# Performance work log

Measured on AMD Instinct MI355X. Metric: run time of the kernel, lower is better.

Reference implementation:

```python
import jax, jax.numpy as jnp
import numpy as np

N, E, G = 50000, 500000, 2000   # nodes, edges, graphs
IN, H, ED, OUT = 64, 128, 16, 1
NUM_GAT = 2                      # num_layers - 1
T = 2                            # num_timesteps


def leaky(x, s=0.01):
    return jnp.where(x >= 0, x, s * x)


def gru_cell(x, h, wih, whh, bih, bhh):
    gi = x @ wih.T + bih
    gh = h @ whh.T + bhh
    ir, iz, inn = jnp.split(gi, 3, -1)
    hr, hz, hn = jnp.split(gh, 3, -1)
    r = jax.nn.sigmoid(ir + hr)
    z = jax.nn.sigmoid(iz + hz)
    n = jnp.tanh(inn + r * hn)
    return (1.0 - z) * n + z * h


def lstm_cell(x, h, c, wih, whh, bih, bhh):
    g = x @ wih.T + bih + h @ whh.T + bhh
    i, f, gg, o = jnp.split(g, 4, -1)
    c2 = jax.nn.sigmoid(f) * c + jax.nn.sigmoid(i) * jnp.tanh(gg)
    h2 = jax.nn.sigmoid(o) * jnp.tanh(c2)
    return h2, c2


def setup_inputs() -> dict:
    key = jax.random.key(0)
    ks = iter(jax.random.split(key, 40))
    def rn(shape, s=0.05):
        return jax.random.normal(next(ks), shape, jnp.float32) * s
    return {
        "x": jax.random.normal(next(ks), (N, IN), jnp.float32),
        "edge_index": jax.random.randint(next(ks), (2, E), 0, N),
        "edge_attr": jax.random.normal(next(ks), (E, ED), jnp.float32),
        "batch": jnp.sort(jax.random.randint(next(ks), (N,), 0, G)),
        "lin1_w": rn((H, IN)), "lin1_b": rn((H,)),
        "nd_lin1_w": rn((H, H + ED)), "nd_lin2_w": rn((H, H)), "nd_bias": rn((H,)),
        "gru0_wih": rn((3 * H, H)), "gru0_whh": rn((3 * H, H)),
        "gru0_bih": rn((3 * H,)), "gru0_bhh": rn((3 * H,)),
        "gat_w": rn((NUM_GAT, H, H)), "gat_asrc": rn((NUM_GAT, H)),
        "gat_adst": rn((NUM_GAT, H)), "gat_b": rn((NUM_GAT, H)),
        "gru_wih": rn((NUM_GAT, 3 * H, H)), "gru_whh": rn((NUM_GAT, 3 * H, H)),
        "gru_bih": rn((NUM_GAT, 3 * H)), "gru_bhh": rn((NUM_GAT, 3 * H)),
        "gin_w": rn((H, H)), "gin_b": rn((H,)),
        "lstm_wih": rn((4 * H, H)), "lstm_whh": rn((4 * H, H)),
        "lstm_bih": rn((4 * H,)), "lstm_bhh": rn((4 * H,)),
        "lin2_w": rn((OUT, H)), "lin2_b": rn((OUT,)),
    }


def reference(x, edge_index, edge_attr, batch,
              lin1_w, lin1_b, nd_lin1_w, nd_lin2_w, nd_bias,
              gru0_wih, gru0_whh, gru0_bih, gru0_bhh,
              gat_w, gat_asrc, gat_adst, gat_b,
              gru_wih, gru_whh, gru_bih, gru_bhh,
              gin_w, gin_b, lstm_wih, lstm_whh, lstm_bih, lstm_bhh,
              lin2_w, lin2_b):
    src, dst = edge_index[0], edge_index[1]  # PyG: messages flow src(j) -> dst(i)
    # input projection
    x1 = leaky(x @ lin1_w.T + lin1_b)
    # nd_conv: gather -> MLP -> scatter-add (dropout=0 in eval)
    m = leaky(jnp.concatenate([x1[src], edge_attr], -1) @ nd_lin1_w.T) @ nd_lin2_w.T
    h = jax.nn.elu(jax.ops.segment_sum(m, dst, num_segments=N) + nd_bias)
    xcur = jax.nn.relu(gru_cell(h, x1, gru0_wih, gru0_whh, gru0_bih, gru0_bhh))
    # GAT layers (heads=1, no self loops, negative_slope=0.01)
    for l in range(NUM_GAT):
        xp = xcur @ gat_w[l].T
        a = leaky(xp[src] @ gat_asrc[l] + xp[dst] @ gat_adst[l], 0.01)
        amax = jax.lax.stop_gradient(jax.ops.segment_max(a, dst, num_segments=N))
        ae = jnp.exp(a - amax[dst])
        denom = jax.ops.segment_sum(ae, dst, num_segments=N)
        alpha = ae / denom[dst]
        h = jax.nn.elu(jax.ops.segment_sum(alpha[:, None] * xp[src], dst, num_segments=N) + gat_b[l])
        xcur = jax.nn.relu(gru_cell(h, xcur,
                                    gru_wih[l], gru_whh[l], gru_bih[l], gru_bhh[l]))
    # global readout: GIN on bipartite (nodes -> graphs) + LSTM refinement
    agg = jax.ops.segment_sum(xcur, batch, num_segments=G)  # [G, H], constant over timesteps
    out = jax.nn.relu(agg)
    for _ in range(T):
        h = jax.nn.elu((out + agg) @ gin_w.T + gin_b)  # GIN eps=0: nn(x_dst + aggr)
        out, _ = lstm_cell(out, h, h, lstm_wih, lstm_whh, lstm_bih, lstm_bhh)
    return out @ lin2_w.T + lin2_b  # [G, OUT]
```

## Files before the change

### kernel.cpp

```cpp
#include <hip/hip_runtime.h>
#include <cstdint>
#include <cmath>

#define NN 50000
#define EE 500000
#define GG 2000

#define DEV __device__ __forceinline__

typedef __attribute__((ext_vector_type(8))) short short8;
typedef __attribute__((ext_vector_type(4))) float floatx4;
typedef _Float16 half2v __attribute__((ext_vector_type(2)));
typedef _Float16 half4v __attribute__((ext_vector_type(4)));
typedef _Float16 half8v __attribute__((ext_vector_type(8)));

DEV float fsig(float x) { return 1.f / (1.f + __expf(-x)); }
DEV float ftanh(float x) {
    const float e = __expf(-2.f * fabsf(x));
    const float t = (1.f - e) / (1.f + e);
    return x >= 0.f ? t : -t;
}

DEV float actf(float x, int act) {
    if (act == 1) return x >= 0.f ? x : 0.01f * x;
    if (act == 2) return x > 0.f ? x : __expf(x) - 1.f;
    if (act == 3) return x > 0.f ? x : 0.f;
    return x;
}

DEV float hdot2(half2v a, half2v b, float c) {
#if __has_builtin(__builtin_amdgcn_fdot2)
    return __builtin_amdgcn_fdot2(a, b, c, false);
#else
    return c + (float)a[0] * (float)b[0] + (float)a[1] * (float)b[1];
#endif
}

#define H2(v, i) __builtin_shufflevector(v, v, 2 * (i), 2 * (i) + 1)

__global__ __launch_bounds__(256) void gemm_f16_k(
    const _Float16* __restrict__ A, const _Float16* __restrict__ W,
    const float* __restrict__ bias, _Float16* __restrict__ C,
    int M, int K, int Nout, int act)
{
    __shared__ unsigned short Als[64 * 136];
    __shared__ unsigned short Bls[64 * 136];
    const int tid = threadIdx.x;
    const int bm = blockIdx.y * 64;
    const int bn = blockIdx.x * 64;

    const int ks = (K == 128) ? 7 : 6;
    const int km = K - 1;
    const int nch = (64 * K) >> 3;
    for (int i = tid; i < nch; i += 256) {
        const int e8 = i << 3;
        const int r = e8 >> ks;
        const int c = e8 & km;
        short8 av = {};
        if (bm + r < M) av = *(const short8*)(A + (size_t)(bm + r) * K + c);
        *(short8*)(Als + r * 136 + c) = av;
        *(short8*)(Bls + r * 136 + c) = *(const short8*)(W + (size_t)(bn + r) * K + c);
    }
    __syncthreads();

    const int wave = tid >> 6;
    const int lane = tid & 63;
    const int wr = (wave >> 1) * 32;
    const int wc = (wave & 1) * 32;
    const int l15 = lane & 15;
    const int quad = lane >> 4;

    floatx4 acc00 = {}, acc01 = {}, acc10 = {}, acc11 = {};
    for (int k0 = 0; k0 < K; k0 += 32) {
        const half8v a0 = *(const half8v*)(Als + (wr + l15) * 136 + k0 + quad * 8);
        const half8v a1 = *(const half8v*)(Als + (wr + 16 + l15) * 136 + k0 + quad * 8);
        const half8v b0 = *(const half8v*)(Bls + (wc + l15) * 136 + k0 + quad * 8);
        const half8v b1 = *(const half8v*)(Bls + (wc + 16 + l15) * 136 + k0 + quad * 8);
        acc00 = __builtin_amdgcn_mfma_f32_16x16x32_f16(a0, b0, acc00, 0, 0, 0);
        acc01 = __builtin_amdgcn_mfma_f32_16x16x32_f16(a0, b1, acc01, 0, 0, 0);
        acc10 = __builtin_amdgcn_mfma_f32_16x16x32_f16(a1, b0, acc10, 0, 0, 0);
        acc11 = __builtin_amdgcn_mfma_f32_16x16x32_f16(a1, b1, acc11, 0, 0, 0);
    }

    const floatx4* accs[4] = { &acc00, &acc01, &acc10, &acc11 };
#pragma unroll
    for (int r = 0; r < 2; ++r) {
#pragma unroll
        for (int c = 0; c < 2; ++c) {
            const floatx4 a = *accs[r * 2 + c];
            const int n = bn + wc + c * 16 + l15;
            const float bv = bias ? bias[n] : 0.f;
#pragma unroll
            for (int i = 0; i < 4; ++i) {
                const int m = bm + wr + r * 16 + quad * 4 + i;
                if (m < M) C[(size_t)m * Nout + n] = (_Float16)actf(a[i] + bv, act);
            }
        }
    }
}

__global__ __launch_bounds__(256) void gemm_dots_k(
    const _Float16* __restrict__ A, const _Float16* __restrict__ W,
    _Float16* __restrict__ C, const float* __restrict__ asrc,
    const float* __restrict__ adst, float* __restrict__ ssrc,
    float* __restrict__ sdst, int M)
{
    __shared__ unsigned short Als[64 * 136];
    __shared__ unsigned short Bls[64 * 136];
    const int tid = threadIdx.x;
    const int bm = blockIdx.y * 64;
    const int bn = blockIdx.x * 64;

    for (int i = tid; i < 1024; i += 256) {
        const int e8 = i << 3;
        const int r = e8 >> 7;
        const int c = e8 & 127;
        short8 av = {};
        if (bm + r < M) av = *(const short8*)(A + (size_t)(bm + r) * 128 + c);
        *(short8*)(Als + r * 136 + c) = av;
        *(short8*)(Bls + r * 136 + c) = *(const short8*)(W + (size_t)(bn + r) * 128 + c);
    }
    __syncthreads();

    const int wave = tid >> 6;
    const int lane = tid & 63;
    const int wr = (wave >> 1) * 32;
    const int wc = (wave & 1) * 32;
    const int l15 = lane & 15;
    const int quad = lane >> 4;

    floatx4 acc00 = {}, acc01 = {}, acc10 = {}, acc11 = {};
    for (int k0 = 0; k0 < 128; k0 += 32) {
        const half8v a0 = *(const half8v*)(Als + (wr + l15) * 136 + k0 + quad * 8);
        const half8v a1 = *(const half8v*)(Als + (wr + 16 + l15) * 136 + k0 + quad * 8);
        const half8v b0 = *(const half8v*)(Bls + (wc + l15) * 136 + k0 + quad * 8);
        const half8v b1 = *(const half8v*)(Bls + (wc + 16 + l15) * 136 + k0 + quad * 8);
        acc00 = __builtin_amdgcn_mfma_f32_16x16x32_f16(a0, b0, acc00, 0, 0, 0);
        acc01 = __builtin_amdgcn_mfma_f32_16x16x32_f16(a0, b1, acc01, 0, 0, 0);
        acc10 = __builtin_amdgcn_mfma_f32_16x16x32_f16(a1, b0, acc10, 0, 0, 0);
        acc11 = __builtin_amdgcn_mfma_f32_16x16x32_f16(a1, b1, acc11, 0, 0, 0);
    }

    const floatx4* accs[4] = { &acc00, &acc01, &acc10, &acc11 };
#pragma unroll
    for (int r = 0; r < 2; ++r)
#pragma unroll
        for (int c = 0; c < 2; ++c) {
            const floatx4 a = *accs[r * 2 + c];
            const int n = bn + wc + c * 16 + l15;
#pragma unroll
            for (int i = 0; i < 4; ++i) {
                const int m = bm + wr + r * 16 + quad * 4 + i;
                if (m < M) C[(size_t)m * 128 + n] = (_Float16)a[i];
            }
        }

    const int n0 = bn + wc + l15;
    const int n1 = n0 + 16;
    const float as0 = asrc[n0], as1 = asrc[n1];
    const float ad0 = adst[n0], ad1 = adst[n1];
#pragma unroll
    for (int r = 0; r < 2; ++r) {
        const floatx4 a0 = r ? acc10 : acc00;
        const floatx4 a1 = r ? acc11 : acc01;
#pragma unroll
        for (int i = 0; i < 4; ++i) {
            float vs = a0[i] * as0 + a1[i] * as1;
            float vd = a0[i] * ad0 + a1[i] * ad1;
            vs += __shfl_down(vs, 8, 16);
            vs += __shfl_down(vs, 4, 16);
            vs += __shfl_down(vs, 2, 16);
            vs += __shfl_down(vs, 1, 16);
            vd += __shfl_down(vd, 8, 16);
            vd += __shfl_down(vd, 4, 16);
            vd += __shfl_down(vd, 2, 16);
            vd += __shfl_down(vd, 1, 16);
            const int m = bm + wr + r * 16 + quad * 4 + i;
            if (l15 == 0 && m < M) {
                atomicAdd(ssrc + m, vs);
                atomicAdd(sdst + m, vd);
            }
        }
    }
}

__global__ __launch_bounds__(256) void lin1p_k(
    const _Float16* __restrict__ xH, const _Float16* __restrict__ lin1_wH,
    const float* __restrict__ lin1_b, const _Float16* __restrict__ nd1wAH,
    _Float16* __restrict__ x1H, _Float16* __restrict__ pH, int M)
{
    __shared__ _Float16 sXin[64 * 72];
    __shared__ _Float16 sX1 [64 * 136];
    const int tid = threadIdx.x;
    const int bm = blockIdx.x * 64;

    for (int i = tid; i < 512; i += 256) {
        const int e8 = i << 3;
        const int r = e8 >> 6;
        const int c = e8 & 63;
        const int m = bm + r;
        half8v v = {};
        if (m < M) v = *(const half8v*)(xH + (size_t)m * 64 + c);
        *(half8v*)(sXin + r * 72 + c) = v;
    }
    __syncthreads();

    const int wave = tid >> 6, lane = tid & 63;
    const int l15 = lane & 15, quad = lane >> 4;
    const int wr = (wave >> 1) * 32;
    const int wc = (wave & 1) * 64;

    {
        floatx4 acc[2][4] = {};
#pragma unroll
        for (int k = 0; k < 2; ++k) {
            half8v a[2];
#pragma unroll
            for (int rf = 0; rf < 2; ++rf)
                a[rf] = *(const half8v*)(sXin + (wr + rf * 16 + l15) * 72 + k * 32 + quad * 8);
#pragma unroll
            for (int ct = 0; ct < 4; ++ct) {
                const half8v b = *(const half8v*)(lin1_wH + (size_t)(wc + ct * 16 + l15) * 64 + k * 32 + quad * 8);
#pragma unroll
                for (int rf = 0; rf < 2; ++rf)
                    acc[rf][ct] = __builtin_amdgcn_mfma_f32_16x16x32_f16(a[rf], b, acc[rf][ct], 0, 0, 0);
            }
        }
#pragma unroll
        for (int rf = 0; rf < 2; ++rf)
#pragma unroll
            for (int ct = 0; ct < 4; ++ct) {
                const int n = wc + ct * 16 + l15;
                const float bv = lin1_b[n];
#pragma unroll
                for (int i = 0; i < 4; ++i) {
                    const int rloc = wr + rf * 16 + quad * 4 + i;
                    float v = acc[rf][ct][i] + bv;
                    v = v >= 0.f ? v : 0.01f * v;
                    const _Float16 h = (_Float16)v;
                    sX1[rloc * 136 + n] = h;
                    const int m = bm + rloc;
                    if (m < M) x1H[(size_t)m * 128 + n] = h;
                }
            }
    }
    __syncthreads();

    {
        floatx4 acc[2][4] = {};
#pragma unroll
        for (int k = 0; k < 4; ++k) {
            half8v a[2];
#pragma unroll
            for (int rf = 0; rf < 2; ++rf)
                a[rf] = *(const half8v*)(sX1 + (wr + rf * 16 + l15) * 136 + k * 32 + quad * 8);
#pragma unroll
            for (int ct = 0; ct < 4; ++ct) {
                const half8v b = *(const half8v*)(nd1wAH + (size_t)(wc + ct * 16 + l15) * 128 + k * 32 + quad * 8);
#pragma unroll
                for (int rf = 0; rf < 2; ++rf)
                    acc[rf][ct] = __builtin_amdgcn_mfma_f32_16x16x32_f16(a[rf], b, acc[rf][ct], 0, 0, 0);
            }
        }
#pragma unroll
        for (int rf = 0; rf < 2; ++rf)
#pragma unroll
            for (int ct = 0; ct < 4; ++ct) {
                const int n = wc + ct * 16 + l15;
#pragma unroll
                for (int i = 0; i < 4; ++i) {
                    const int m = bm + wr + rf * 16 + quad * 4 + i;
                    if (m < M) pH[(size_t)m * 128 + n] = (_Float16)acc[rf][ct][i];
                }
            }
    }
}

__global__ __launch_bounds__(256, 4) void gru_fused4_k(
    const _Float16* __restrict__ xin, const _Float16* __restrict__ hin,
    const _Float16* __restrict__ wih, const _Float16* __restrict__ whh,
    const float* __restrict__ bih, const float* __restrict__ bhh,
    _Float16* __restrict__ xout, int M)
{
    __shared__ unsigned short sX[64 * 136];
    __shared__ unsigned short sH[64 * 136];

    const int tid = threadIdx.x;
    const int bm = blockIdx.x * 64;

    for (int i = tid; i < 1024; i += 256) {
        const int e8 = i << 3;
        const int r = e8 >> 7;
        const int c = e8 & 127;
        const int m = bm + r;
        short8 xv = {}, hv = {};
        if (m < M) {
            xv = *(const short8*)(xin + (size_t)m * 128 + c);
            hv = *(const short8*)(hin + (size_t)m * 128 + c);
        }
        *(short8*)(sX + r * 136 + c) = xv;
        *(short8*)(sH + r * 136 + c) = hv;
    }
    __syncthreads();

    const int wave = tid >> 6;
    const int lane = tid & 63;
    const int l15 = lane & 15;
    const int quad = lane >> 4;
    const int j0 = (blockIdx.y * 4 + wave) * 16;
    const int j = j0 + l15;

    const float br  = bih[j] + bhh[j];
    const float bz  = bih[128 + j] + bhh[128 + j];
    const float bni = bih[256 + j];
    const float bnh = bhh[256 + j];

    floatx4 aR[4] = {}, aZ[4] = {}, aNi[4] = {}, aNh[4] = {};

#pragma unroll
    for (int k = 0; k < 4; ++k) {
        const size_t wrow = (size_t)(j0 + l15) * 128 + k * 32 + quad * 8;
        const half8v wri = *(const half8v*)(wih + wrow);
        const half8v wzi = *(const half8v*)(wih + 128 * 128 + wrow);
        const half8v wni = *(const half8v*)(wih + 2 * 128 * 128 + wrow);
        const half8v wrh = *(const half8v*)(whh + wrow);
        const half8v wzh = *(const half8v*)(whh + 128 * 128 + wrow);
        const half8v wnh = *(const half8v*)(whh + 2 * 128 * 128 + wrow);
#pragma unroll
        for (int rf = 0; rf < 4; ++rf) {
            const half8v ax = *(const half8v*)(sX + (rf * 16 + l15) * 136 + k * 32 + quad * 8);
            const half8v ah = *(const half8v*)(sH + (rf * 16 + l15) * 136 + k * 32 + quad * 8);
            aR[rf]  = __builtin_amdgcn_mfma_f32_16x16x32_f16(ax, wri, aR[rf], 0, 0, 0);
            aR[rf]  = __builtin_amdgcn_mfma_f32_16x16x32_f16(ah, wrh, aR[rf], 0, 0, 0);
            aZ[rf]  = __builtin_amdgcn_mfma_f32_16x16x32_f16(ax, wzi, aZ[rf], 0, 0, 0);
            aZ[rf]  = __builtin_amdgcn_mfma_f32_16x16x32_f16(ah, wzh, aZ[rf], 0, 0, 0);
            aNi[rf] = __builtin_amdgcn_mfma_f32_16x16x32_f16(ax, wni, aNi[rf], 0, 0, 0);
            aNh[rf] = __builtin_amdgcn_mfma_f32_16x16x32_f16(ah, wnh, aNh[rf], 0, 0, 0);
        }
    }

#pragma unroll
    for (int rf = 0; rf < 4; ++rf) {
#pragma unroll
        for (int i = 0; i < 4; ++i) {
            const int m = bm + rf * 16 + quad * 4 + i;
            if (m >= M) continue;
            const float rg = fsig(aR[rf][i] + br);
            const float zg = fsig(aZ[rf][i] + bz);
            const float ng = ftanh(aNi[rf][i] + bni + rg * (aNh[rf][i] + bnh));
            const float hp = (float)((const _Float16*)sH)[(rf * 16 + quad * 4 + i) * 136 + j];
            const float v = (1.f - zg) * ng + zg * hp;
            xout[(size_t)m * 128 + j] = (_Float16)(v > 0.f ? v : 0.f);
        }
    }
}

__global__ void hist_k(const int* __restrict__ ei, int* __restrict__ deg, int E)
{
    int e = blockIdx.x * 256 + threadIdx.x;
    if (e >= E) return;
    atomicAdd(deg + ei[E + e], 1);
}

__global__ __launch_bounds__(1024) void scan_part_k(const int* __restrict__ deg,
                                                    int* __restrict__ bsum, int n)
{
    __shared__ int sh[1024];
    const int t = threadIdx.x;
    const int i = blockIdx.x * 1024 + t;
    sh[t] = (i < n) ? deg[i] : 0;
    __syncthreads();
#pragma unroll
    for (int off = 512; off; off >>= 1) {
        if (t < off) sh[t] += sh[t + off];
        __syncthreads();
    }
    if (t == 0) bsum[blockIdx.x] = sh[0];
}

__global__ void scan_tops_k(const int* __restrict__ bsum, int* __restrict__ boff,
                            int nb, int* __restrict__ rowptr, int n)
{
    if (threadIdx.x != 0 || blockIdx.x != 0) return;
    int run = 0;
    for (int b = 0; b < nb; ++b) { boff[b] = run; run += bsum[b]; }
    rowptr[n] = run;
}

__global__ __launch_bounds__(1024) void scan_final_k(const int* __restrict__ deg,
                                                     const int* __restrict__ boff,
                                                     int* __restrict__ rowptr, int n)
{
    __shared__ int sh[1024];
    const int t = threadIdx.x;
    const int i = blockIdx.x * 1024 + t;
    const int v = (i < n) ? deg[i] : 0;
    sh[t] = v;
    __syncthreads();
#pragma unroll
    for (int off = 1; off < 1024; off <<= 1) {
        int add = (t >= off) ? sh[t - off] : 0;
        __syncthreads();
        sh[t] += add;
        __syncthreads();
    }
    if (i < n) rowptr[i] = boff[blockIdx.x] + sh[t] - v;
}

__global__ void fill_csr_k(const int* __restrict__ ei, const int* __restrict__ rowptr,
                           int* __restrict__ cursor, int* __restrict__ csr_src,
                           int* __restrict__ csr_eid, int E)
{
    int e = blockIdx.x * 256 + threadIdx.x;
    if (e >= E) return;
    int s = ei[e], d = ei[E + e];
    int pos = atomicAdd(cursor + d, 1);
    int slot = rowptr[d] + pos;
    csr_src[slot] = s;
    csr_eid[slot] = e;
}

__global__ void gptr_k(const int* __restrict__ batch, int* __restrict__ gptr,
                       int N, int G)
{
    int n = blockIdx.x * 256 + threadIdx.x;
    if (n >= N) return;
    if (n == 0) {
        for (int g = 0; g <= batch[0]; ++g) gptr[g] = 0;
    } else {
        const int a = batch[n - 1], b = batch[n];
        for (int g = a + 1; g <= b; ++g) gptr[g] = n;
    }
    if (n == N - 1) {
        for (int g = batch[N - 1] + 1; g <= G; ++g) gptr[g] = N;
    }
}

__global__ __launch_bounds__(128) void graph_sum_k(
    const _Float16* __restrict__ xc, const int* __restrict__ gptr,
    _Float16* __restrict__ aggH)
{
    const int g = blockIdx.x;
    const int t = threadIdx.x;
    const int n0 = gptr[g], n1 = gptr[g + 1];
    float acc = 0.f;
    for (int n = n0; n < n1; ++n) acc += (float)xc[(size_t)n * 128 + t];
    aggH[(size_t)g * 128 + t] = (_Float16)acc;
}

struct CvtSeg { const float* src; _Float16* dst; int n; };
struct CvtArgs { CvtSeg s[12]; int count; };

__global__ void cvt_multi_k(CvtArgs a)
{
    const int seg = blockIdx.y;
    if (seg >= a.count) return;
    const CvtSeg cs = a.s[seg];
    for (int i = blockIdx.x * 256 + threadIdx.x; i < cs.n; i += gridDim.x * 256)
        cs.dst[i] = (_Float16)cs.src[i];
}

__global__ void cvt_ndwA_k(const float* __restrict__ ndw, _Float16* __restrict__ outp)
{
    int t = blockIdx.x * 256 + threadIdx.x;
    if (t >= 16384) return;
    int r = t >> 7, c = t & 127;
    outp[r * 128 + c] = (_Float16)ndw[r * 144 + c];
}

__global__ void cvt_ndwB_k(const float* __restrict__ ndw, _Float16* __restrict__ outp)
{
    int t = blockIdx.x * 256 + threadIdx.x;
    if (t >= 2048) return;
    int r = t >> 4, k = t & 15;
    outp[r * 16 + k] = (_Float16)ndw[r * 144 + 128 + k];
}

__global__ __launch_bounds__(128) void nd_gather_k(
    const int* __restrict__ rowptr, const int* __restrict__ csr_src,
    const int* __restrict__ csr_eid, const _Float16* __restrict__ eaH,
    const _Float16* __restrict__ wH, const _Float16* __restrict__ pH,
    _Float16* __restrict__ outp)
{
    __shared__ float racc[4][128];
    const int d = blockIdx.x;
    const int t = threadIdx.x;
    const int g  = t >> 5;
    const int fq = t & 31;

    half8v w0[4], w1[4];
#pragma unroll
    for (int f = 0; f < 4; ++f) {
        w0[f] = *(const half8v*)(wH + (fq * 4 + f) * 16);
        w1[f] = *(const half8v*)(wH + (fq * 4 + f) * 16 + 8);
    }

    const int b0 = rowptr[d], b1 = rowptr[d + 1];
    float acc[4] = {};
    for (int i = b0 + g; i < b1; i += 4) {
        const int s = csr_src[i], e = csr_eid[i];
        const half8v e0 = *(const half8v*)(eaH + (size_t)e * 16);
        const half8v e1 = *(const half8v*)(eaH + (size_t)e * 16 + 8);
        const half4v p4 = *(const half4v*)(pH + (size_t)s * 128 + fq * 4);
#pragma unroll
        for (int f = 0; f < 4; ++f) {
            float q = 0.f;
            q = hdot2(H2(e0, 0), H2(w0[f], 0), q);
            q = hdot2(H2(e0, 1), H2(w0[f], 1), q);
            q = hdot2(H2(e0, 2), H2(w0[f], 2), q);
            q = hdot2(H2(e0, 3), H2(w0[f], 3), q);
            q = hdot2(H2(e1, 0), H2(w1[f], 0), q);
            q = hdot2(H2(e1, 1), H2(w1[f], 1), q);
            q = hdot2(H2(e1, 2), H2(w1[f], 2), q);
            q = hdot2(H2(e1, 3), H2(w1[f], 3), q);
            const float v = (float)p4[f] + q;
            acc[f] += v >= 0.f ? v : 0.01f * v;
        }
    }
#pragma unroll
    for (int f = 0; f < 4; ++f) racc[g][fq * 4 + f] = acc[f];
    __syncthreads();

    outp[(size_t)d * 128 + t] =
        (_Float16)(racc[0][t] + racc[1][t] + racc[2][t] + racc[3][t]);
}

__global__ __launch_bounds__(128) void gat_gather_k(
    const int* __restrict__ rowptr, const int* __restrict__ csr_src,
    const float* __restrict__ ssrc, const float* __restrict__ sdst,
    const _Float16* __restrict__ xp, const float* __restrict__ bias,
    _Float16* __restrict__ outp)
{
    const int d = blockIdx.x;
    const int t = threadIdx.x;
    __shared__ float red[128];
    __shared__ float lw[128];
    __shared__ int   ls[128];
    __shared__ float racc[4][128];

    const int b0 = rowptr[d], b1 = rowptr[d + 1];
    const int deg = b1 - b0;
    const float sdd = sdst[d];

    const int g  = t >> 5;
    const int fq = t & 31;
    float4 acc = make_float4(0.f, 0.f, 0.f, 0.f);
    float dpart = 0.f;
    for (int base = b0; base < b1; base += 128) {
        const int len = min(128, b1 - base);
        if (t < len) {
            const int s = csr_src[base + t];
            float a = ssrc[s] + sdd;
            a = a >= 0.f ? a : 0.01f * a;
            const float w = __expf(a);
            lw[t] = w;
            ls[t] = s;
            dpart += w;
        }
        __syncthreads();
        for (int j = 0; j < len; j += 4) {
            const int jj = j + g;
            if (jj < len) {
                const float w = lw[jj];
                const half4v hv = *(const half4v*)(xp + (size_t)ls[jj] * 128 + fq * 4);
                acc.x += w * (float)hv[0];
                acc.y += w * (float)hv[1];
                acc.z += w * (float)hv[2];
                acc.w += w * (float)hv[3];
            }
        }
        __syncthreads();
    }

    red[t] = dpart;
    __syncthreads();
#pragma unroll
    for (int off = 64; off; off >>= 1) {
        if (t < off) red[t] += red[t + off];
        __syncthreads();
    }
    const float denom = red[0];

    racc[g][fq * 4 + 0] = acc.x;
    racc[g][fq * 4 + 1] = acc.y;
    racc[g][fq * 4 + 2] = acc.z;
    racc[g][fq * 4 + 3] = acc.w;
    __syncthreads();

    const float s4 = racc[0][t] + racc[1][t] + racc[2][t] + racc[3][t];
    float v = (deg > 0 ? s4 / denom : 0.f) + bias[t];
    outp[(size_t)d * 128 + t] = (_Float16)(v > 0.f ? v : __expf(v) - 1.f);
}

__global__ __launch_bounds__(256) void gin_lstm_k(
    const _Float16* __restrict__ aggH,
    const _Float16* __restrict__ ginw, const float* __restrict__ ginb,
    const _Float16* __restrict__ lwih, const _Float16* __restrict__ lwhh,
    const float* __restrict__ lbih, const float* __restrict__ lbhh,
    const float* __restrict__ l2w, const float* __restrict__ l2b,
    float* __restrict__ y, int G)
{
    __shared__ _Float16 sOa[16 * 136];
    __shared__ _Float16 sOb[16 * 136];
    __shared__ _Float16 sG [16 * 136];
    __shared__ _Float16 sT [16 * 136];
    __shared__ float    sC [16 * 128];

    const int tid = threadIdx.x, wave = tid >> 6, lane = tid & 63;
    const int l15 = lane & 15, quad = lane >> 4;
    const int g0 = blockIdx.x * 16;

    {
        const int r = tid >> 4;
        const int c = (tid & 15) * 8;
        half8v v = {};
        if (g0 + r < G) v = *(const half8v*)(aggH + (size_t)(g0 + r) * 128 + c);
        *(half8v*)(sG + r * 136 + c) = v;
        half8v rv;
#pragma unroll
        for (int i = 0; i < 8; ++i) rv[i] = (float)v[i] > 0.f ? v[i] : (_Float16)0.f;
        *(half8v*)(sOa + r * 136 + c) = rv;
    }
    __syncthreads();

    _Float16* sIn = sOa;
    _Float16* sOut = sOb;
#pragma unroll
    for (int ts = 0; ts < 2; ++ts) {
        for (int ci = 0; ci < 2; ++ci) {
            const int j0 = (wave * 2 + ci) * 16;
            floatx4 acc = {};
#pragma unroll
            for (int k = 0; k < 4; ++k) {
                const half8v b = *(const half8v*)(ginw + (size_t)(j0 + l15) * 128 + k * 32 + quad * 8);
                const half8v a = *(const half8v*)(sIn + l15 * 136 + k * 32 + quad * 8)
                               + *(const half8v*)(sG  + l15 * 136 + k * 32 + quad * 8);
                acc = __builtin_amdgcn_mfma_f32_16x16x32_f16(a, b, acc, 0, 0, 0);
            }
            const int j = j0 + l15;
            const float bg = ginb[j];
#pragma unroll
            for (int i = 0; i < 4; ++i) {
                const int row = quad * 4 + i;
                float v = acc[i] + bg;
                v = v > 0.f ? v : __expf(v) - 1.f;
                sT[row * 136 + j] = (_Float16)v;
                sC[row * 128 + j] = v;
            }
        }
        __syncthreads();

        for (int ci = 0; ci < 2; ++ci) {
            const int j0 = (wave * 2 + ci) * 16;
            floatx4 acc[4] = {};
#pragma unroll
            for (int k = 0; k < 4; ++k) {
                const half8v ao = *(const half8v*)(sIn + l15 * 136 + k * 32 + quad * 8);
                const half8v ah = *(const half8v*)(sT  + l15 * 136 + k * 32 + quad * 8);
#pragma unroll
                for (int gt = 0; gt < 4; ++gt) {
                    const half8v bw = *(const half8v*)(lwih + (size_t)(gt * 128 + j0 + l15) * 128 + k * 32 + quad * 8);
                    const half8v bh = *(const half8v*)(lwhh + (size_t)(gt * 128 + j0 + l15) * 128 + k * 32 + quad * 8);
                    acc[gt] = __builtin_amdgcn_mfma_f32_16x16x32_f16(ao, bw, acc[gt], 0, 0, 0);
                    acc[gt] = __builtin_amdgcn_mfma_f32_16x16x32_f16(ah, bh, acc[gt], 0, 0, 0);
                }
            }
            const int j = j0 + l15;
            const float bi_ = lbih[j]       + lbhh[j];
            const float bf_ = lbih[128 + j] + lbhh[128 + j];
            const float bgg = lbih[256 + j] + lbhh[256 + j];
            const float bo_ = lbih[384 + j] + lbhh[384 + j];
#pragma unroll
            for (int i = 0; i < 4; ++i) {
                const int row = quad * 4 + i;
                const float hg = sC[row * 128 + j];
                const float c2 = fsig(acc[1][i] + bf_) * hg
                               + fsig(acc[0][i] + bi_) * ftanh(acc[2][i] + bgg);
                const float on = fsig(acc[3][i] + bo_) * ftanh(c2);
                sOut[row * 136 + j] = (_Float16)on;
            }
        }
        __syncthreads();
        _Float16* tmp = sIn; sIn = sOut; sOut = tmp;
    }

    if (tid < 64) {
        const int r = tid >> 2;
        const int part = tid & 3;
        float v = 0.f;
        for (int j = part * 32; j < part * 32 + 32; ++j)
            v += (float)sIn[r * 136 + j] * l2w[j];
        v += __shfl_down(v, 2);
        v += __shfl_down(v, 1);
        if (part == 0 && g0 + r < G) y[g0 + r] = v + l2b[0];
    }
}


extern "C" void kernel_launch(void* const* d_in, const int* in_sizes, int n_in,
                              void* d_out, int out_size, void* d_ws, size_t ws_size,
                              hipStream_t stream)
{
    const float* x      = (const float*)d_in[0];
    const int*   ei     = (const int*)  d_in[1];
    const float* ea     = (const float*)d_in[2];
    const int*   batch  = (const int*)  d_in[3];
    const float* lin1_w = (const float*)d_in[4];
    const float* lin1_b = (const float*)d_in[5];
    const float* nd1w   = (const float*)d_in[6];
    const float* nd2w   = (const float*)d_in[7];
    const float* ndb    = (const float*)d_in[8];
    const float* g0wih  = (const float*)d_in[9];
    const float* g0whh  = (const float*)d_in[10];
    const float* g0bih  = (const float*)d_in[11];
    const float* g0bhh  = (const float*)d_in[12];
    const float* gatw   = (const float*)d_in[13];
    const float* gatas  = (const float*)d_in[14];
    const float* gatad  = (const float*)d_in[15];
    const float* gatb   = (const float*)d_in[16];
    const float* gwih   = (const float*)d_in[17];
    const float* gwhh   = (const float*)d_in[18];
    const float* gbih   = (const float*)d_in[19];
    const float* gbhh   = (const float*)d_in[20];
    const float* ginw   = (const float*)d_in[21];
    const float* ginb   = (const float*)d_in[22];
    const float* lwih   = (const float*)d_in[23];
    const float* lwhh   = (const float*)d_in[24];
    const float* lbih   = (const float*)d_in[25];
    const float* lbhh   = (const float*)d_in[26];
    const float* l2w    = (const float*)d_in[27];
    const float* l2b    = (const float*)d_in[28];
    float* outp = (float*)d_out;

    const int N = NN, E = EE, G = GG;
    const int Npad = (N + 63) & ~63;

    float* ws = (float*)d_ws;
    size_t off = 0;
    auto alloc = [&](size_t n) {
        float* r = ws + off;
        off += (n + 63) & ~(size_t)63;
        return r;
    };
    _Float16* xH    = (_Float16*)alloc((size_t)N * 32);
    _Float16* x1H   = (_Float16*)alloc((size_t)N * 64);
    _Float16* hbufH = (_Float16*)alloc((size_t)N * 64);
    _Float16* accbH = (_Float16*)alloc((size_t)N * 64);
    _Float16* xcH   = (_Float16*)alloc((size_t)N * 64);
    _Float16* pH    = (_Float16*)alloc((size_t)N * 64);
    _Float16* eaH   = (_Float16*)alloc((size_t)E * 8);
    _Float16* aggH  = (_Float16*)alloc((size_t)G * 64);
    _Float16* lin1_wH = (_Float16*)alloc(4096);
    _Float16* nd1wAH  = (_Float16*)alloc(8192);
    _Float16* ndwBH   = (_Float16*)alloc(1024);
    _Float16* nd2wH   = (_Float16*)alloc(8192);
    _Float16* g0wihH  = (_Float16*)alloc(24576);
    _Float16* g0whhH  = (_Float16*)alloc(24576);
    _Float16* gwihH   = (_Float16*)alloc(49152);
    _Float16* gwhhH   = (_Float16*)alloc(49152);
    _Float16* gatwH   = (_Float16*)alloc(16384);
    _Float16* ginwH   = (_Float16*)alloc(8192);
    _Float16* lwihH   = (_Float16*)alloc(32768);
    _Float16* lwhhH   = (_Float16*)alloc(32768);
    float* ssrcA = alloc((size_t)N);
    float* sdstA = alloc((size_t)N);
    float* ssrcB = alloc((size_t)N);
    float* sdstB = alloc((size_t)N);
    int* deg     = (int*)alloc((size_t)N);
    int* rowptr  = (int*)alloc((size_t)N + 1);
    int* cursor  = (int*)alloc((size_t)N);
    int* bsum    = (int*)alloc(64);
    int* boff    = (int*)alloc(64);
    int* csr_src = (int*)alloc((size_t)E);
    int* csr_eid = (int*)alloc((size_t)E);
    int* gptr    = (int*)alloc((size_t)G + 1);
    (void)ws_size;

    auto gemmh = [&](const _Float16* A, const _Float16* W, const float* bias,
                     _Float16* C, int M, int K, int Nout, int act) {
        dim3 grid(Nout / 64, (M + 63) / 64);
        gemm_f16_k<<<grid, 256, 0, stream>>>(A, W, bias, C, M, K, Nout, act);
    };
    auto nb = [](int n) { return (n + 255) / 256; };

    auto gru = [&](const _Float16* xin, const _Float16* hin,
                   const _Float16* wih, const _Float16* whh,
                   const float* bih, const float* bhh, _Float16* xout) {
        dim3 grid((N + 63) / 64, 2);
        gru_fused4_k<<<grid, 256, 0, stream>>>(
            xin, hin, wih, whh, bih, bhh, xout, N);
    };

    hipMemsetAsync(deg, 0, (size_t)N * 4, stream);
    hipMemsetAsync(cursor, 0, (size_t)N * 4, stream);
    hipMemsetAsync(ssrcA, 0, (size_t)Npad * 4 * 4, stream);
    hist_k<<<nb(E), 256, 0, stream>>>(ei, deg, E);
    const int nblk = (N + 1023) / 1024;
    scan_part_k<<<nblk, 1024, 0, stream>>>(deg, bsum, N);
    scan_tops_k<<<1, 64, 0, stream>>>(bsum, boff, nblk, rowptr, N);
    scan_final_k<<<nblk, 1024, 0, stream>>>(deg, boff, rowptr, N);
    fill_csr_k<<<nb(E), 256, 0, stream>>>(ei, rowptr, cursor, csr_src, csr_eid, E);
    gptr_k<<<nb(N), 256, 0, stream>>>(batch, gptr, N, G);

    CvtArgs ca;
    ca.s[0]  = { ea,     eaH,     E * 16 };
    ca.s[1]  = { x,      xH,      N * 64 };
    ca.s[2]  = { lin1_w, lin1_wH, 8192 };
    ca.s[3]  = { nd2w,   nd2wH,   16384 };
    ca.s[4]  = { g0wih,  g0wihH,  49152 };
    ca.s[5]  = { g0whh,  g0whhH,  49152 };
    ca.s[6]  = { gwih,   gwihH,   98304 };
    ca.s[7]  = { gwhh,   gwhhH,   98304 };
    ca.s[8]  = { gatw,   gatwH,   32768 };
    ca.s[9]  = { ginw,   ginwH,   16384 };
    ca.s[10] = { lwih,   lwihH,   65536 };
    ca.s[11] = { lwhh,   lwhhH,   65536 };
    ca.count = 12;
    cvt_multi_k<<<dim3(2048, 12), 256, 0, stream>>>(ca);
    cvt_ndwA_k<<<64, 256, 0, stream>>>(nd1w, nd1wAH);
    cvt_ndwB_k<<<8, 256, 0, stream>>>(nd1w, ndwBH);

    lin1p_k<<<(N + 63) / 64, 256, 0, stream>>>(
        xH, lin1_wH, lin1_b, nd1wAH, x1H, pH, N);

    nd_gather_k<<<N, 128, 0, stream>>>(rowptr, csr_src, csr_eid, eaH, ndwBH, pH, accbH);
    gemmh(accbH, nd2wH, ndb, hbufH, N, 128, 128, 2);

    gru(hbufH, x1H, g0wihH, g0whhH, g0bih, g0bhh, xcH);

    const _Float16* xcur = xcH;
    _Float16* xnext = x1H;
    for (int l = 0; l < 2; ++l) {
        float* ss = l ? ssrcB : ssrcA;
        float* sd = l ? sdstB : sdstA;
        dim3 grid(2, (N + 63) / 64);
        gemm_dots_k<<<grid, 256, 0, stream>>>(
            xcur, gatwH + (size_t)l * 16384, pH,
            gatas + l * 128, gatad + l * 128, ss, sd, N);
        gat_gather_k<<<N, 128, 0, stream>>>(rowptr, csr_src, ss, sd, pH,
                                            gatb + l * 128, hbufH);
        gru(hbufH, xcur, gwihH + (size_t)l * 49152, gwhhH + (size_t)l * 49152,
            gbih + l * 384, gbhh + l * 384, xnext);
        const _Float16* t = xcur; xcur = xnext; xnext = (_Float16*)t;
    }

    graph_sum_k<<<G, 128, 0, stream>>>(xcur, gptr, aggH);

    gin_lstm_k<<<(G + 15) / 16, 256, 0, stream>>>(
        aggH, ginwH, ginb, lwihH, lwhhH, lbih, lbhh, l2w, l2b, outp, G);
}
```

Baseline: 639.8 us.

## Permute edge attributes into CSR order during fill and simplify nd gather

The CSR fill kernel now converts edge attributes to fp16 and writes them at each edge's CSR slot. This removes the csr_eid indirection and the separate ea conversion pass. The nd gather kernel is restructured so each thread owns one feature and walks edges sequentially, reading contiguous edge attributes and prefetching the next source row. The 4-way shared-memory reduction disappears, but each thread now evaluates a 16-wide dot per edge redundantly across threads, and the edge loop is serial per block.

```diff
diff --git a/kernel.cpp b/kernel.cpp
--- a/kernel.cpp
+++ b/kernel.cpp
@@ -407,9 +407,9 @@
     if (i < n) rowptr[i] = boff[blockIdx.x] + sh[t] - v;
 }
 
-__global__ void fill_csr_k(const int* __restrict__ ei, const int* __restrict__ rowptr,
-                           int* __restrict__ cursor, int* __restrict__ csr_src,
-                           int* __restrict__ csr_eid, int E)
+__global__ void fill_csr_k(const int* __restrict__ ei, const float* __restrict__ ea,
+                           const int* __restrict__ rowptr, int* __restrict__ cursor,
+                           int* __restrict__ csr_src, _Float16* __restrict__ eaP, int E)
 {
     int e = blockIdx.x * 256 + threadIdx.x;
     if (e >= E) return;
@@ -417,7 +417,17 @@
     int pos = atomicAdd(cursor + d, 1);
     int slot = rowptr[d] + pos;
     csr_src[slot] = s;
-    csr_eid[slot] = e;
+    const float4 a0 = *(const float4*)(ea + (size_t)e * 16);
+    const float4 a1 = *(const float4*)(ea + (size_t)e * 16 + 4);
+    const float4 a2 = *(const float4*)(ea + (size_t)e * 16 + 8);
+    const float4 a3 = *(const float4*)(ea + (size_t)e * 16 + 12);
+    half8v h0, h1;
+    h0[0] = (_Float16)a0.x; h0[1] = (_Float16)a0.y; h0[2] = (_Float16)a0.z; h0[3] = (_Float16)a0.w;
+    h0[4] = (_Float16)a1.x; h0[5] = (_Float16)a1.y; h0[6] = (_Float16)a1.z; h0[7] = (_Float16)a1.w;
+    h1[0] = (_Float16)a2.x; h1[1] = (_Float16)a2.y; h1[2] = (_Float16)a2.z; h1[3] = (_Float16)a2.w;
+    h1[4] = (_Float16)a3.x; h1[5] = (_Float16)a3.y; h1[6] = (_Float16)a3.z; h1[7] = (_Float16)a3.w;
+    *(half8v*)(eaP + (size_t)slot * 16) = h0;
+    *(half8v*)(eaP + (size_t)slot * 16 + 8) = h1;
 }
 
 __global__ void gptr_k(const int* __restrict__ batch, int* __restrict__ gptr,
@@ -478,51 +488,37 @@
 
 __global__ __launch_bounds__(128) void nd_gather_k(
     const int* __restrict__ rowptr, const int* __restrict__ csr_src,
-    const int* __restrict__ csr_eid, const _Float16* __restrict__ eaH,
-    const _Float16* __restrict__ wH, const _Float16* __restrict__ pH,
-    _Float16* __restrict__ outp)
-{
-    __shared__ float racc[4][128];
+    const _Float16* __restrict__ eaP, const _Float16* __restrict__ wH,
+    const _Float16* __restrict__ pH, _Float16* __restrict__ outp)
+{
     const int d = blockIdx.x;
     const int t = threadIdx.x;
-    const int g  = t >> 5;
-    const int fq = t & 31;
-
-    half8v w0[4], w1[4];
-#pragma unroll
-    for (int f = 0; f < 4; ++f) {
-        w0[f] = *(const half8v*)(wH + (fq * 4 + f) * 16);
-        w1[f] = *(const half8v*)(wH + (fq * 4 + f) * 16 + 8);
-    }
+    const half8v w0 = *(const half8v*)(wH + t * 16);
+    const half8v w1 = *(const half8v*)(wH + t * 16 + 8);
 
     const int b0 = rowptr[d], b1 = rowptr[d + 1];
-    float acc[4] = {};
-    for (int i = b0 + g; i < b1; i += 4) {
-        const int s = csr_src[i], e = csr_eid[i];
-        const half8v e0 = *(const half8v*)(eaH + (size_t)e * 16);
-        const half8v e1 = *(const half8v*)(eaH + (size_t)e * 16 + 8);
-        const half4v p4 = *(const half4v*)(pH + (size_t)s * 128 + fq * 4);
-#pragma unroll
-        for (int f = 0; f < 4; ++f) {
-            float q = 0.f;
-            q = hdot2(H2(e0, 0), H2(w0[f], 0), q);
-            q = hdot2(H2(e0, 1), H2(w0[f], 1), q);
-            q = hdot2(H2(e0, 2), H2(w0[f], 2), q);
-            q = hdot2(H2(e0, 3), H2(w0[f], 3), q);
-            q = hdot2(H2(e1, 0), H2(w1[f], 0), q);
-            q = hdot2(H2(e1, 1), H2(w1[f], 1), q);
-            q = hdot2(H2(e1, 2), H2(w1[f], 2), q);
-            q = hdot2(H2(e1, 3), H2(w1[f], 3), q);
-            const float v = (float)p4[f] + q;
-            acc[f] += v >= 0.f ? v : 0.01f * v;
-        }
-    }
-#pragma unroll
-    for (int f = 0; f < 4; ++f) racc[g][fq * 4 + f] = acc[f];
-    __syncthreads();
-
-    outp[(size_t)d * 128 + t] =
-        (_Float16)(racc[0][t] + racc[1][t] + racc[2][t] + racc[3][t]);
+    float acc = 0.f;
+    float pv = 0.f;
+    if (b0 < b1) pv = (float)pH[(size_t)csr_src[b0] * 128 + t];
+    for (int i = b0; i < b1; ++i) {
+        float npv = 0.f;
+        if (i + 1 < b1) npv = (float)pH[(size_t)csr_src[i + 1] * 128 + t];
+        const half8v e0 = *(const half8v*)(eaP + (size_t)i * 16);
+        const half8v e1 = *(const half8v*)(eaP + (size_t)i * 16 + 8);
+        float q = 0.f;
+        q = hdot2(H2(e0, 0), H2(w0, 0), q);
+        q = hdot2(H2(e0, 1), H2(w0, 1), q);
+        q = hdot2(H2(e0, 2), H2(w0, 2), q);
+        q = hdot2(H2(e0, 3), H2(w0, 3), q);
+        q = hdot2(H2(e1, 0), H2(w1, 0), q);
+        q = hdot2(H2(e1, 1), H2(w1, 1), q);
+        q = hdot2(H2(e1, 2), H2(w1, 2), q);
+        q = hdot2(H2(e1, 3), H2(w1, 3), q);
+        const float v = pv + q;
+        acc += v >= 0.f ? v : 0.01f * v;
+        pv = npv;
+    }
+    outp[(size_t)d * 128 + t] = (_Float16)acc;
 }
 
 __global__ __launch_bounds__(128) void gat_gather_k(
@@ -748,7 +744,7 @@
     _Float16* accbH = (_Float16*)alloc((size_t)N * 64);
     _Float16* xcH   = (_Float16*)alloc((size_t)N * 64);
     _Float16* pH    = (_Float16*)alloc((size_t)N * 64);
-    _Float16* eaH   = (_Float16*)alloc((size_t)E * 8);
+    _Float16* eaP   = (_Float16*)alloc((size_t)E * 8);
     _Float16* aggH  = (_Float16*)alloc((size_t)G * 64);
     _Float16* lin1_wH = (_Float16*)alloc(4096);
     _Float16* nd1wAH  = (_Float16*)alloc(8192);
@@ -772,7 +768,6 @@
     int* bsum    = (int*)alloc(64);
     int* boff    = (int*)alloc(64);
     int* csr_src = (int*)alloc((size_t)E);
-    int* csr_eid = (int*)alloc((size_t)E);
     int* gptr    = (int*)alloc((size_t)G + 1);
     (void)ws_size;
 
@@ -799,31 +794,30 @@
     scan_part_k<<<nblk, 1024, 0, stream>>>(deg, bsum, N);
     scan_tops_k<<<1, 64, 0, stream>>>(bsum, boff, nblk, rowptr, N);
     scan_final_k<<<nblk, 1024, 0, stream>>>(deg, boff, rowptr, N);
-    fill_csr_k<<<nb(E), 256, 0, stream>>>(ei, rowptr, cursor, csr_src, csr_eid, E);
+    fill_csr_k<<<nb(E), 256, 0, stream>>>(ei, ea, rowptr, cursor, csr_src, eaP, E);
     gptr_k<<<nb(N), 256, 0, stream>>>(batch, gptr, N, G);
 
     CvtArgs ca;
-    ca.s[0]  = { ea,     eaH,     E * 16 };
-    ca.s[1]  = { x,      xH,      N * 64 };
-    ca.s[2]  = { lin1_w, lin1_wH, 8192 };
-    ca.s[3]  = { nd2w,   nd2wH,   16384 };
-    ca.s[4]  = { g0wih,  g0wihH,  49152 };
-    ca.s[5]  = { g0whh,  g0whhH,  49152 };
-    ca.s[6]  = { gwih,   gwihH,   98304 };
-    ca.s[7]  = { gwhh,   gwhhH,   98304 };
-    ca.s[8]  = { gatw,   gatwH,   32768 };
-    ca.s[9]  = { ginw,   ginwH,   16384 };
-    ca.s[10] = { lwih,   lwihH,   65536 };
-    ca.s[11] = { lwhh,   lwhhH,   65536 };
-    ca.count = 12;
-    cvt_multi_k<<<dim3(2048, 12), 256, 0, stream>>>(ca);
+    ca.s[0]  = { x,      xH,      N * 64 };
+    ca.s[1]  = { lin1_w, lin1_wH, 8192 };
+    ca.s[2]  = { nd2w,   nd2wH,   16384 };
+    ca.s[3]  = { g0wih,  g0wihH,  49152 };
+    ca.s[4]  = { g0whh,  g0whhH,  49152 };
+    ca.s[5]  = { gwih,   gwihH,   98304 };
+    ca.s[6]  = { gwhh,   gwhhH,   98304 };
+    ca.s[7]  = { gatw,   gatwH,   32768 };
+    ca.s[8]  = { ginw,   ginwH,   16384 };
+    ca.s[9]  = { lwih,   lwihH,   65536 };
+    ca.s[10] = { lwhh,   lwhhH,   65536 };
+    ca.count = 11;
+    cvt_multi_k<<<dim3(2048, 11), 256, 0, stream>>>(ca);
     cvt_ndwA_k<<<64, 256, 0, stream>>>(nd1w, nd1wAH);
     cvt_ndwB_k<<<8, 256, 0, stream>>>(nd1w, ndwBH);
 
     lin1p_k<<<(N + 63) / 64, 256, 0, stream>>>(
         xH, lin1_wH, lin1_b, nd1wAH, x1H, pH, N);
 
-    nd_gather_k<<<N, 128, 0, stream>>>(rowptr, csr_src, csr_eid, eaH, ndwBH, pH, accbH);
+    nd_gather_k<<<N, 128, 0, stream>>>(rowptr, csr_src, eaP, ndwBH, pH, accbH);
     gemmh(accbH, nd2wH, ndb, hbufH, N, 128, 128, 2);
 
     gru(hbufH, x1H, g0wihH, g0whhH, g0bih, g0bhh, xcH);
```

Measured after the change: 596.2 us. 1.07x faster.
